# Performance work log

Hardware: AMD Instinct MI355X
Metric: run time of the kernel (lower is better)

The kernel has to match this reference:

```python
import jax, jax.numpy as jnp
import numpy as np

N_NODES = 100000   # vertices
N_EDGES = 20000    # hyperedges
NNZ = 1600000      # incidence entries (avg vertex degree 16)
D_IN = 128
D_OUT = 128


def setup_inputs() -> dict:
    key = jax.random.key(0)
    k1, k2, k3, k4, k5 = jax.random.split(key, 5)
    X = jax.random.normal(k1, (N_NODES, D_IN), dtype=jnp.float32)
    v_idx = jax.random.randint(k2, (NNZ,), 0, N_NODES)
    e_idx = jax.random.randint(k3, (NNZ,), 0, N_EDGES)
    theta_w = jax.random.normal(k4, (D_IN, D_OUT), dtype=jnp.float32) / np.sqrt(D_IN)
    theta_b = jax.random.normal(k5, (D_OUT,), dtype=jnp.float32) * 0.01
    return {"X": X, "theta_w": theta_w, "theta_b": theta_b,
            "v_idx": v_idx, "e_idx": e_idx}


def reference(X, theta_w, theta_b, v_idx, e_idx):
    # degrees (edge weights w_e = 1)
    ones = jnp.ones(v_idx.shape[0], dtype=X.dtype)
    d_v = jax.ops.segment_sum(ones, v_idx, num_segments=N_NODES)   # [N]
    d_e = jax.ops.segment_sum(ones, e_idx, num_segments=N_EDGES)   # [M]
    inv_sqrt_dv = jnp.where(d_v > 0, d_v ** -0.5, 0.0)
    inv_de = jnp.where(d_e > 0, 1.0 / d_e, 0.0)

    # theta: dense GEMM
    Xt = X @ theta_w + theta_b                                     # [N, D_OUT]

    # smoothing_with_HGNN: D_v^{-1/2} H W D_e^{-1} H^T D_v^{-1/2} Xt
    Xs = Xt * inv_sqrt_dv[:, None]                                 # [N, D_OUT]
    Ye = jax.ops.segment_sum(Xs[v_idx], e_idx, num_segments=N_EDGES)  # H^T Xs -> [M, D_OUT]
    Ye = Ye * inv_de[:, None]
    Xv = jax.ops.segment_sum(Ye[e_idx], v_idx, num_segments=N_NODES)  # H Ye -> [N, D_OUT]
    return jax.nn.relu(Xv * inv_sqrt_dv[:, None])
```

## Files before the change

kernel.cpp:

```cpp
#include <hip/hip_runtime.h>

#define N_NODES 100000
#define N_EDGES 20000
#define NNZ     1600000
#define D       128
#define DW      64

#define NB      256
#define CAP_E   8192
#define CAP_V   8192
#define SPAN_E  ((N_EDGES + NB - 1) / NB)
#define SPAN_V  ((N_NODES + NB - 1) / NB)
#define P1_CHUNK 8192
#define P1_BLOCKS ((NNZ + P1_CHUNK - 1) / P1_CHUNK)

__device__ __forceinline__ unsigned int pack_bf2(float lo, float hi) {
  unsigned int ul = __float_as_uint(lo), uh = __float_as_uint(hi);
  ul = (ul + 0x7FFFu + ((ul >> 16) & 1u)) >> 16;
  uh = (uh + 0x7FFFu + ((uh >> 16) & 1u)) & 0xFFFF0000u;
  return ul | uh;
}

__global__ void k_init(int* __restrict__ ce, int* __restrict__ cv) {
  int t = threadIdx.x;
  ce[t] = t * CAP_E;
  cv[t] = t * CAP_V;
}

__global__ __launch_bounds__(256) void k_bin(const int* __restrict__ v_idx, const int* __restrict__ e_idx,
                                             int* __restrict__ ce, int* __restrict__ cv,
                                             unsigned int* __restrict__ Te, unsigned int* __restrict__ Tv) {
  __shared__ int he[NB], hv[NB], be[NB], bv[NB], le[NB], lv[NB];
  int t = threadIdx.x;
  he[t] = 0; hv[t] = 0; le[t] = 0; lv[t] = 0;
  __syncthreads();
  int base = blockIdx.x * P1_CHUNK;
  int v[32], e[32];
#pragma unroll
  for (int j = 0; j < 32; ++j) {
    int idx = base + j * 256 + t;
    if (idx < NNZ) {
      v[j] = v_idx[idx]; e[j] = e_idx[idx];
      atomicAdd(&he[e[j] / SPAN_E], 1);
      atomicAdd(&hv[v[j] / SPAN_V], 1);
    } else v[j] = -1;
  }
  __syncthreads();
  be[t] = he[t] ? atomicAdd(&ce[t], he[t]) : 0;
  bv[t] = hv[t] ? atomicAdd(&cv[t], hv[t]) : 0;
  __syncthreads();
#pragma unroll
  for (int j = 0; j < 32; ++j) {
    if (v[j] < 0) continue;
    int eb = e[j] / SPAN_E, vb = v[j] / SPAN_V;
    int se = be[eb] + atomicAdd(&le[eb], 1);
    int sv = bv[vb] + atomicAdd(&lv[vb], 1);
    if (se < (eb + 1) * CAP_E) Te[se] = ((unsigned)e[j] << 17) | (unsigned)v[j];
    if (sv < (vb + 1) * CAP_V) Tv[sv] = ((unsigned)v[j] << 15) | (unsigned)e[j];
  }
}

__global__ __launch_bounds__(256) void k_sort_e(const int* __restrict__ ce, unsigned int* __restrict__ Te,
                                                int* __restrict__ cnt_e, float* __restrict__ invde,
                                                int* __restrict__ starts_e) {
  __shared__ unsigned int raw[CAP_E];
  __shared__ int hist[SPAN_E], lcur[SPAN_E], loff[SPAN_E + 1];
  int b = blockIdx.x, t = threadIdx.x;
  int e0 = b * SPAN_E;
  int span = N_EDGES - e0; if (span > SPAN_E) span = SPAN_E;
  if (span <= 0) return;
  int n = ce[b] - b * CAP_E; if (n > CAP_E) n = CAP_E; if (n < 0) n = 0;
  for (int i = t; i < n; i += 256) raw[i] = Te[b * CAP_E + i];
  for (int i = t; i < span; i += 256) { hist[i] = 0; lcur[i] = 0; }
  __syncthreads();
  for (int i = t; i < n; i += 256) atomicAdd(&hist[(int)(raw[i] >> 17) - e0], 1);
  __syncthreads();
  if (t == 0) { int run = 0; for (int i = 0; i < span; ++i) { loff[i] = run; run += hist[i]; } loff[span] = run; }
  __syncthreads();
  for (int i = t; i < n; i += 256) {
    unsigned int p = raw[i];
    int l = (int)(p >> 17) - e0;
    int slot = loff[l] + atomicAdd(&lcur[l], 1);
    Te[b * CAP_E + slot] = p & 0x1FFFFu;
  }
  for (int i = t; i < span; i += 256) {
    int d = hist[i];
    cnt_e[e0 + i] = d;
    invde[e0 + i] = d > 0 ? 1.0f / (float)d : 0.0f;
    starts_e[e0 + i] = b * CAP_E + loff[i];
  }
}

__global__ __launch_bounds__(256) void k_sort_v(const int* __restrict__ cv, unsigned int* __restrict__ Tv,
                                                int* __restrict__ cnt_v, float* __restrict__ risv,
                                                int* __restrict__ starts_v) {
  __shared__ unsigned int raw[CAP_V];
  __shared__ int hist[SPAN_V], lcur[SPAN_V], loff[SPAN_V + 1];
  int b = blockIdx.x, t = threadIdx.x;
  int v0 = b * SPAN_V;
  int span = N_NODES - v0; if (span > SPAN_V) span = SPAN_V;
  if (span <= 0) return;
  int n = cv[b] - b * CAP_V; if (n > CAP_V) n = CAP_V; if (n < 0) n = 0;
  for (int i = t; i < n; i += 256) raw[i] = Tv[b * CAP_V + i];
  for (int i = t; i < span; i += 256) { hist[i] = 0; lcur[i] = 0; }
  __syncthreads();
  for (int i = t; i < n; i += 256) atomicAdd(&hist[(int)(raw[i] >> 15) - v0], 1);
  __syncthreads();
  if (t == 0) { int run = 0; for (int i = 0; i < span; ++i) { loff[i] = run; run += hist[i]; } loff[span] = run; }
  __syncthreads();
  for (int i = t; i < n; i += 256) {
    unsigned int p = raw[i];
    int l = (int)(p >> 15) - v0;
    int slot = loff[l] + atomicAdd(&lcur[l], 1);
    Tv[b * CAP_V + slot] = p & 0x7FFFu;
  }
  for (int i = t; i < span; i += 256) {
    int d = hist[i];
    cnt_v[v0 + i] = d;
    risv[v0 + i] = d > 0 ? rsqrtf((float)d) : 0.0f;
    starts_v[v0 + i] = b * CAP_V + loff[i];
  }
}

__global__ __launch_bounds__(256) void k_prescale(const float* __restrict__ X, const float* __restrict__ risv,
                                                  unsigned int* __restrict__ Xs) {
  int p = blockIdx.x * 256 + threadIdx.x;
  if (p >= N_NODES * DW) return;
  int v = p >> 6;
  float r = risv[v];
  float2 x = *(const float2*)(X + (size_t)p * 2);
  Xs[p] = pack_bf2(r * x.x, r * x.y);
}

__global__ void k_edge_gather(const unsigned int* __restrict__ Xs, const float* __restrict__ risv,
                              const int* __restrict__ starts_e, const int* __restrict__ cnt_e,
                              const unsigned int* __restrict__ members,
                              float* __restrict__ Qe, float* __restrict__ qv) {
  int wid = (blockIdx.x * 256 + threadIdx.x) >> 6;
  int lane = threadIdx.x & 63;
  if (wid >= N_EDGES) return;
  int beg = __builtin_amdgcn_readfirstlane(starts_e[wid]);
  int end = beg + __builtin_amdgcn_readfirstlane(cnt_e[wid]);
  float ax = 0.f, ay = 0.f, q = 0.f;
  int i = beg;
  for (; i + 8 <= end; i += 8) {
    int vv[8]; unsigned int xx[8];
#pragma unroll
    for (int j = 0; j < 8; ++j) vv[j] = members[i + j];
#pragma unroll
    for (int j = 0; j < 8; ++j) xx[j] = Xs[(size_t)vv[j] * DW + lane];
#pragma unroll
    for (int j = 0; j < 8; ++j) q += risv[vv[j]];
#pragma unroll
    for (int j = 0; j < 8; ++j) {
      ax += __uint_as_float(xx[j] << 16);
      ay += __uint_as_float(xx[j] & 0xFFFF0000u);
    }
  }
  for (; i < end; ++i) {
    int v = members[i];
    unsigned int x = Xs[(size_t)v * DW + lane];
    ax += __uint_as_float(x << 16);
    ay += __uint_as_float(x & 0xFFFF0000u);
    q += risv[v];
  }
  float2 o; o.x = ax; o.y = ay;
  *(float2*)(Qe + (size_t)wid * D + lane * 2) = o;
  if (lane == 0) qv[wid] = q;
}

__global__ __launch_bounds__(256) void k_gemm(const float* __restrict__ Qe, const float* __restrict__ qv,
                                              const float* __restrict__ W, const float* __restrict__ bias,
                                              const float* __restrict__ invde, unsigned int* __restrict__ Yeb) {
  __shared__ float Wl[D * D];
  __shared__ float bl[D];
  __shared__ float Ql[16][130];
  int tid = threadIdx.x;
  const float4* W4 = (const float4*)W;
  float4* Wl4 = (float4*)Wl;
#pragma unroll
  for (int j = 0; j < 16; ++j) Wl4[tid + 256 * j] = W4[tid + 256 * j];
  if (tid < 32) ((float4*)bl)[tid] = ((const float4*)bias)[tid];
  int row0 = blockIdx.x * 16;
  const float4* Q4 = (const float4*)(Qe + (size_t)row0 * D);
#pragma unroll
  for (int j = 0; j < 2; ++j) {
    int idx = tid + 256 * j;
    int r = idx >> 5, c4 = idx & 31;
    float4 val = Q4[idx];
    Ql[r][c4 * 4 + 0] = val.x; Ql[r][c4 * 4 + 1] = val.y;
    Ql[r][c4 * 4 + 2] = val.z; Ql[r][c4 * 4 + 3] = val.w;
  }
  __syncthreads();
  int ty = tid >> 4, tx = tid & 15;
  float acc[8];
#pragma unroll
  for (int j = 0; j < 8; ++j) acc[j] = 0.f;
#pragma unroll 4
  for (int k = 0; k < D; ++k) {
    float xv = Ql[ty][k];
    const float* wr = Wl + k * D + tx * 8;
#pragma unroll
    for (int j = 0; j < 8; ++j) acc[j] += xv * wr[j];
  }
  int row = row0 + ty;
  float s = invde[row]; float q = qv[row];
  unsigned int* orow = Yeb + (size_t)row * DW + tx * 4;
#pragma unroll
  for (int j = 0; j < 4; ++j) {
    float lo = s * (acc[2 * j]     + q * bl[tx * 8 + 2 * j]);
    float hi = s * (acc[2 * j + 1] + q * bl[tx * 8 + 2 * j + 1]);
    orow[j] = pack_bf2(lo, hi);
  }
}

__global__ void k_vertex_gather(const unsigned int* __restrict__ Yeb, const float* __restrict__ risv,
                                const int* __restrict__ starts_v, const int* __restrict__ cnt_v,
                                const unsigned int* __restrict__ members,
                                float* __restrict__ out) {
  int wid = (blockIdx.x * 256 + threadIdx.x) >> 6;
  int lane = threadIdx.x & 63;
  if (wid >= N_NODES) return;
  int beg = __builtin_amdgcn_readfirstlane(starts_v[wid]);
  int end = beg + __builtin_amdgcn_readfirstlane(cnt_v[wid]);
  float ax = 0.f, ay = 0.f;
  int i = beg;
  for (; i + 4 <= end; i += 4) {
    int e0 = members[i], e1 = members[i + 1], e2 = members[i + 2], e3 = members[i + 3];
    unsigned int y0 = Yeb[(size_t)e0 * DW + lane];
    unsigned int y1 = Yeb[(size_t)e1 * DW + lane];
    unsigned int y2 = Yeb[(size_t)e2 * DW + lane];
    unsigned int y3 = Yeb[(size_t)e3 * DW + lane];
    ax += __uint_as_float(y0 << 16) + __uint_as_float(y1 << 16)
        + __uint_as_float(y2 << 16) + __uint_as_float(y3 << 16);
    ay += __uint_as_float(y0 & 0xFFFF0000u) + __uint_as_float(y1 & 0xFFFF0000u)
        + __uint_as_float(y2 & 0xFFFF0000u) + __uint_as_float(y3 & 0xFFFF0000u);
  }
  for (; i < end; ++i) {
    int e = members[i];
    unsigned int y = Yeb[(size_t)e * DW + lane];
    ax += __uint_as_float(y << 16);
    ay += __uint_as_float(y & 0xFFFF0000u);
  }
  float s = risv[wid];
  float2 o; o.x = fmaxf(ax * s, 0.f); o.y = fmaxf(ay * s, 0.f);
  *(float2*)(out + (size_t)wid * D + lane * 2) = o;
}

extern "C" void kernel_launch(void* const* d_in, const int* in_sizes, int n_in,
                              void* d_out, int out_size, void* d_ws, size_t ws_size,
                              hipStream_t stream) {
  const float* X    = (const float*)d_in[0];
  const float* W    = (const float*)d_in[1];
  const float* bias = (const float*)d_in[2];
  const int* v_idx  = (const int*)d_in[3];
  const int* e_idx  = (const int*)d_in[4];
  float* out = (float*)d_out;

  char* p = (char*)d_ws;
  auto alloc = [&](size_t bytes) { char* r = p; p += (bytes + 255) & ~(size_t)255; return r; };
  unsigned int* Te  = (unsigned int*)alloc((size_t)NB * CAP_E * 4);
  unsigned int* Tv  = (unsigned int*)alloc((size_t)NB * CAP_V * 4);
  unsigned int* Xs  = (unsigned int*)alloc((size_t)N_NODES * DW * 4);
  unsigned int* Yeb = (unsigned int*)alloc((size_t)N_EDGES * DW * 4);
  float* Qe    = (float*)alloc((size_t)N_EDGES * D * 4);
  float* qv    = (float*)alloc((size_t)N_EDGES * 4);
  float* risv  = (float*)alloc((size_t)N_NODES * 4);
  float* invde = (float*)alloc((size_t)N_EDGES * 4);
  int* cnt_e    = (int*)alloc((size_t)N_EDGES * 4);
  int* cnt_v    = (int*)alloc((size_t)N_NODES * 4);
  int* starts_e = (int*)alloc((size_t)N_EDGES * 4);
  int* starts_v = (int*)alloc((size_t)N_NODES * 4);
  int* ce       = (int*)alloc(NB * 4);
  int* cv       = (int*)alloc(NB * 4);

  k_init<<<1, NB, 0, stream>>>(ce, cv);
  k_bin<<<P1_BLOCKS, 256, 0, stream>>>(v_idx, e_idx, ce, cv, Te, Tv);
  k_sort_e<<<NB, 256, 0, stream>>>(ce, Te, cnt_e, invde, starts_e);
  k_sort_v<<<NB, 256, 0, stream>>>(cv, Tv, cnt_v, risv, starts_v);
  k_prescale<<<(N_NODES * DW + 255) / 256, 256, 0, stream>>>(X, risv, Xs);

  k_edge_gather<<<N_EDGES / 4, 256, 0, stream>>>(Xs, risv, starts_e, cnt_e, Te, Qe, qv);
  k_gemm<<<N_EDGES / 16, 256, 0, stream>>>(Qe, qv, W, bias, invde, Yeb);
  k_vertex_gather<<<N_NODES / 4, 256, 0, stream>>>(Yeb, risv, starts_v, cnt_v, Tv, out);
}
```

Baseline: 309.0 us.

## Move qv sum into edge sort, store Qe as bf16, deepen gather unrolls

```diff
diff --git a/kernel.cpp b/kernel.cpp
--- a/kernel.cpp
+++ b/kernel.cpp
@@ -57,37 +57,6 @@
     int sv = bv[vb] + atomicAdd(&lv[vb], 1);
     if (se < (eb + 1) * CAP_E) Te[se] = ((unsigned)e[j] << 17) | (unsigned)v[j];
     if (sv < (vb + 1) * CAP_V) Tv[sv] = ((unsigned)v[j] << 15) | (unsigned)e[j];
-  }
-}
-
-__global__ __launch_bounds__(256) void k_sort_e(const int* __restrict__ ce, unsigned int* __restrict__ Te,
-                                                int* __restrict__ cnt_e, float* __restrict__ invde,
-                                                int* __restrict__ starts_e) {
-  __shared__ unsigned int raw[CAP_E];
-  __shared__ int hist[SPAN_E], lcur[SPAN_E], loff[SPAN_E + 1];
-  int b = blockIdx.x, t = threadIdx.x;
-  int e0 = b * SPAN_E;
-  int span = N_EDGES - e0; if (span > SPAN_E) span = SPAN_E;
-  if (span <= 0) return;
-  int n = ce[b] - b * CAP_E; if (n > CAP_E) n = CAP_E; if (n < 0) n = 0;
-  for (int i = t; i < n; i += 256) raw[i] = Te[b * CAP_E + i];
-  for (int i = t; i < span; i += 256) { hist[i] = 0; lcur[i] = 0; }
-  __syncthreads();
-  for (int i = t; i < n; i += 256) atomicAdd(&hist[(int)(raw[i] >> 17) - e0], 1);
-  __syncthreads();
-  if (t == 0) { int run = 0; for (int i = 0; i < span; ++i) { loff[i] = run; run += hist[i]; } loff[span] = run; }
-  __syncthreads();
-  for (int i = t; i < n; i += 256) {
-    unsigned int p = raw[i];
-    int l = (int)(p >> 17) - e0;
-    int slot = loff[l] + atomicAdd(&lcur[l], 1);
-    Te[b * CAP_E + slot] = p & 0x1FFFFu;
-  }
-  for (int i = t; i < span; i += 256) {
-    int d = hist[i];
-    cnt_e[e0 + i] = d;
-    invde[e0 + i] = d > 0 ? 1.0f / (float)d : 0.0f;
-    starts_e[e0 + i] = b * CAP_E + loff[i];
   }
 }
 
@@ -122,6 +91,43 @@
   }
 }
 
+__global__ __launch_bounds__(256) void k_sort_e(const int* __restrict__ ce, unsigned int* __restrict__ Te,
+                                                const float* __restrict__ risv,
+                                                int* __restrict__ cnt_e, float* __restrict__ invde,
+                                                int* __restrict__ starts_e, float* __restrict__ qv) {
+  __shared__ unsigned int raw[CAP_E];
+  __shared__ int hist[SPAN_E], lcur[SPAN_E], loff[SPAN_E + 1];
+  __shared__ float qacc[SPAN_E];
+  int b = blockIdx.x, t = threadIdx.x;
+  int e0 = b * SPAN_E;
+  int span = N_EDGES - e0; if (span > SPAN_E) span = SPAN_E;
+  if (span <= 0) return;
+  int n = ce[b] - b * CAP_E; if (n > CAP_E) n = CAP_E; if (n < 0) n = 0;
+  for (int i = t; i < n; i += 256) raw[i] = Te[b * CAP_E + i];
+  for (int i = t; i < span; i += 256) { hist[i] = 0; lcur[i] = 0; qacc[i] = 0.f; }
+  __syncthreads();
+  for (int i = t; i < n; i += 256) atomicAdd(&hist[(int)(raw[i] >> 17) - e0], 1);
+  __syncthreads();
+  if (t == 0) { int run = 0; for (int i = 0; i < span; ++i) { loff[i] = run; run += hist[i]; } loff[span] = run; }
+  __syncthreads();
+  for (int i = t; i < n; i += 256) {
+    unsigned int p = raw[i];
+    int l = (int)(p >> 17) - e0;
+    int vtx = (int)(p & 0x1FFFFu);
+    int slot = loff[l] + atomicAdd(&lcur[l], 1);
+    Te[b * CAP_E + slot] = (unsigned)vtx;
+    atomicAdd(&qacc[l], risv[vtx]);
+  }
+  __syncthreads();
+  for (int i = t; i < span; i += 256) {
+    int d = hist[i];
+    cnt_e[e0 + i] = d;
+    invde[e0 + i] = d > 0 ? 1.0f / (float)d : 0.0f;
+    starts_e[e0 + i] = b * CAP_E + loff[i];
+    qv[e0 + i] = qacc[i];
+  }
+}
+
 __global__ __launch_bounds__(256) void k_prescale(const float* __restrict__ X, const float* __restrict__ risv,
                                                   unsigned int* __restrict__ Xs) {
   int p = blockIdx.x * 256 + threadIdx.x;
@@ -132,44 +138,51 @@
   Xs[p] = pack_bf2(r * x.x, r * x.y);
 }
 
-__global__ void k_edge_gather(const unsigned int* __restrict__ Xs, const float* __restrict__ risv,
+__global__ void k_edge_gather(const unsigned int* __restrict__ Xs,
                               const int* __restrict__ starts_e, const int* __restrict__ cnt_e,
                               const unsigned int* __restrict__ members,
-                              float* __restrict__ Qe, float* __restrict__ qv) {
+                              unsigned int* __restrict__ Qeb) {
   int wid = (blockIdx.x * 256 + threadIdx.x) >> 6;
   int lane = threadIdx.x & 63;
   if (wid >= N_EDGES) return;
   int beg = __builtin_amdgcn_readfirstlane(starts_e[wid]);
   int end = beg + __builtin_amdgcn_readfirstlane(cnt_e[wid]);
-  float ax = 0.f, ay = 0.f, q = 0.f;
+  float ax = 0.f, ay = 0.f;
   int i = beg;
-  for (; i + 8 <= end; i += 8) {
+  for (; i + 16 <= end; i += 16) {
+    int vv[16]; unsigned int xx[16];
+#pragma unroll
+    for (int j = 0; j < 16; ++j) vv[j] = members[i + j];
+#pragma unroll
+    for (int j = 0; j < 16; ++j) xx[j] = Xs[(size_t)vv[j] * DW + lane];
+#pragma unroll
+    for (int j = 0; j < 16; ++j) {
+      ax += __uint_as_float(xx[j] << 16);
+      ay += __uint_as_float(xx[j] & 0xFFFF0000u);
+    }
+  }
+  if (i + 8 <= end) {
     int vv[8]; unsigned int xx[8];
 #pragma unroll
     for (int j = 0; j < 8; ++j) vv[j] = members[i + j];
 #pragma unroll
     for (int j = 0; j < 8; ++j) xx[j] = Xs[(size_t)vv[j] * DW + lane];
-#pragma unroll
-    for (int j = 0; j < 8; ++j) q += risv[vv[j]];
 #pragma unroll
     for (int j = 0; j < 8; ++j) {
       ax += __uint_as_float(xx[j] << 16);
       ay += __uint_as_float(xx[j] & 0xFFFF0000u);
     }
+    i += 8;
   }
   for (; i < end; ++i) {
-    int v = members[i];
-    unsigned int x = Xs[(size_t)v * DW + lane];
+    unsigned int x = Xs[(size_t)members[i] * DW + lane];
     ax += __uint_as_float(x << 16);
     ay += __uint_as_float(x & 0xFFFF0000u);
-    q += risv[v];
-  }
-  float2 o; o.x = ax; o.y = ay;
-  *(float2*)(Qe + (size_t)wid * D + lane * 2) = o;
-  if (lane == 0) qv[wid] = q;
-}
-
-__global__ __launch_bounds__(256) void k_gemm(const float* __restrict__ Qe, const float* __restrict__ qv,
+  }
+  Qeb[(size_t)wid * DW + lane] = pack_bf2(ax, ay);
+}
+
+__global__ __launch_bounds__(256) void k_gemm(const unsigned int* __restrict__ Qeb, const float* __restrict__ qv,
                                               const float* __restrict__ W, const float* __restrict__ bias,
                                               const float* __restrict__ invde, unsigned int* __restrict__ Yeb) {
   __shared__ float Wl[D * D];
@@ -182,14 +195,14 @@
   for (int j = 0; j < 16; ++j) Wl4[tid + 256 * j] = W4[tid + 256 * j];
   if (tid < 32) ((float4*)bl)[tid] = ((const float4*)bias)[tid];
   int row0 = blockIdx.x * 16;
-  const float4* Q4 = (const float4*)(Qe + (size_t)row0 * D);
-#pragma unroll
-  for (int j = 0; j < 2; ++j) {
+  const unsigned int* Q8 = Qeb + (size_t)row0 * DW;
+#pragma unroll
+  for (int j = 0; j < 4; ++j) {
     int idx = tid + 256 * j;
-    int r = idx >> 5, c4 = idx & 31;
-    float4 val = Q4[idx];
-    Ql[r][c4 * 4 + 0] = val.x; Ql[r][c4 * 4 + 1] = val.y;
-    Ql[r][c4 * 4 + 2] = val.z; Ql[r][c4 * 4 + 3] = val.w;
+    int r = idx >> 6, c = idx & 63;
+    unsigned int u = Q8[idx];
+    Ql[r][2 * c]     = __uint_as_float(u << 16);
+    Ql[r][2 * c + 1] = __uint_as_float(u & 0xFFFF0000u);
   }
   __syncthreads();
   int ty = tid >> 4, tx = tid & 15;
@@ -225,20 +238,20 @@
   int end = beg + __builtin_amdgcn_readfirstlane(cnt_v[wid]);
   float ax = 0.f, ay = 0.f;
   int i = beg;
-  for (; i + 4 <= end; i += 4) {
-    int e0 = members[i], e1 = members[i + 1], e2 = members[i + 2], e3 = members[i + 3];
-    unsigned int y0 = Yeb[(size_t)e0 * DW + lane];
-    unsigned int y1 = Yeb[(size_t)e1 * DW + lane];
-    unsigned int y2 = Yeb[(size_t)e2 * DW + lane];
-    unsigned int y3 = Yeb[(size_t)e3 * DW + lane];
-    ax += __uint_as_float(y0 << 16) + __uint_as_float(y1 << 16)
-        + __uint_as_float(y2 << 16) + __uint_as_float(y3 << 16);
-    ay += __uint_as_float(y0 & 0xFFFF0000u) + __uint_as_float(y1 & 0xFFFF0000u)
-        + __uint_as_float(y2 & 0xFFFF0000u) + __uint_as_float(y3 & 0xFFFF0000u);
+  for (; i + 8 <= end; i += 8) {
+    int ee[8]; unsigned int yy[8];
+#pragma unroll
+    for (int j = 0; j < 8; ++j) ee[j] = members[i + j];
+#pragma unroll
+    for (int j = 0; j < 8; ++j) yy[j] = Yeb[(size_t)ee[j] * DW + lane];
+#pragma unroll
+    for (int j = 0; j < 8; ++j) {
+      ax += __uint_as_float(yy[j] << 16);
+      ay += __uint_as_float(yy[j] & 0xFFFF0000u);
+    }
   }
   for (; i < end; ++i) {
-    int e = members[i];
-    unsigned int y = Yeb[(size_t)e * DW + lane];
+    unsigned int y = Yeb[(size_t)members[i] * DW + lane];
     ax += __uint_as_float(y << 16);
     ay += __uint_as_float(y & 0xFFFF0000u);
   }
@@ -262,8 +275,8 @@
   unsigned int* Te  = (unsigned int*)alloc((size_t)NB * CAP_E * 4);
   unsigned int* Tv  = (unsigned int*)alloc((size_t)NB * CAP_V * 4);
   unsigned int* Xs  = (unsigned int*)alloc((size_t)N_NODES * DW * 4);
+  unsigned int* Qeb = (unsigned int*)alloc((size_t)N_EDGES * DW * 4);
   unsigned int* Yeb = (unsigned int*)alloc((size_t)N_EDGES * DW * 4);
-  float* Qe    = (float*)alloc((size_t)N_EDGES * D * 4);
   float* qv    = (float*)alloc((size_t)N_EDGES * 4);
   float* risv  = (float*)alloc((size_t)N_NODES * 4);
   float* invde = (float*)alloc((size_t)N_EDGES * 4);
@@ -276,11 +289,11 @@
 
   k_init<<<1, NB, 0, stream>>>(ce, cv);
   k_bin<<<P1_BLOCKS, 256, 0, stream>>>(v_idx, e_idx, ce, cv, Te, Tv);
-  k_sort_e<<<NB, 256, 0, stream>>>(ce, Te, cnt_e, invde, starts_e);
   k_sort_v<<<NB, 256, 0, stream>>>(cv, Tv, cnt_v, risv, starts_v);
+  k_sort_e<<<NB, 256, 0, stream>>>(ce, Te, risv, cnt_e, invde, starts_e, qv);
   k_prescale<<<(N_NODES * DW + 255) / 256, 256, 0, stream>>>(X, risv, Xs);
 
-  k_edge_gather<<<N_EDGES / 4, 256, 0, stream>>>(Xs, risv, starts_e, cnt_e, Te, Qe, qv);
-  k_gemm<<<N_EDGES / 16, 256, 0, stream>>>(Qe, qv, W, bias, invde, Yeb);
+  k_edge_gather<<<N_EDGES / 4, 256, 0, stream>>>(Xs, starts_e, cnt_e, Te, Qeb);
+  k_gemm<<<N_EDGES / 16, 256, 0, stream>>>(Qeb, qv, W, bias, invde, Yeb);
   k_vertex_gather<<<N_NODES / 4, 256, 0, stream>>>(Yeb, risv, starts_v, cnt_v, Tv, out);
 }
```

Measured after the change: 307.6 us. About the same (-0.5%).
